# Kernel tuning notes

Measured on AMD Instinct MI355X. Metric: run time of the kernel, lower is better.

## Reference

```python
import jax, jax.numpy as jnp
import numpy as np

B, G, L, S = 4096, 16000, 64, 20000  # batch spots, genes, labels, total spots
LOG_2PI = float(np.log(2.0 * np.pi))


def _log_nb_positive_altparam(x, r, o):
    # NB with total_count r > 0 and logits o (stereoscope parametrization)
    return (jax.lax.lgamma(x + r) - jax.lax.lgamma(r) - jax.lax.lgamma(x + 1.0)
            + x * jax.nn.log_sigmoid(o) + r * jax.nn.log_sigmoid(-o))


def setup_inputs() -> dict:
    key = jax.random.key(0)
    ks = jax.random.split(key, 8)
    x = jax.random.randint(ks[0], (B, G), 0, 100, dtype=jnp.int32)
    y = jax.random.randint(ks[1], (B, 1), 0, L, dtype=jnp.int32)
    ind_x = jax.random.randint(ks[2], (B, 1), 0, S, dtype=jnp.int32)
    W = jax.random.normal(ks[3], (G, L), dtype=jnp.float32)          # fixed dictionary
    px_o = 0.5 * jax.random.normal(ks[4], (G,), dtype=jnp.float32)   # fixed log-odds
    eta = jax.random.normal(ks[5], (G,), dtype=jnp.float32)
    V = jax.random.normal(ks[6], (L + 1, S), dtype=jnp.float32)
    beta = 0.1 * jax.random.normal(ks[7], (G,), dtype=jnp.float32)
    return {"x": x, "y": y, "ind_x": ind_x, "W": W, "px_o": px_o,
            "eta": eta, "V": V, "beta": beta}


def reference(x, y, ind_x, W, px_o, eta, V, beta):
    x_f = x.astype(jnp.float32)                      # [B, G]
    beta_sp = jax.nn.softplus(beta)                  # [G]
    w_sp = jax.nn.softplus(W)                        # [G, L]
    eps_sp = jax.nn.softplus(eta)                    # [G]
    # r_hat = [beta*W | eps]  -> [G, L+1]
    r_hat = jnp.concatenate([beta_sp[:, None] * w_sp, eps_sp[:, None]], axis=1)
    # column-gather from V (embedding lookup over spots), then softplus
    v_ind = jax.nn.softplus(V[:, ind_x[:, 0]])       # [L+1, B]
    # thin matmul, inner dim L+1; px_rate: [B, G]
    px_rate = jnp.einsum("gl,lb->bg", r_hat, v_ind)
    # NB reconstruction loss per spot
    reconst_loss = -jnp.sum(_log_nb_positive_altparam(x_f, px_rate, px_o[None, :]), axis=-1)  # [B]
    # -sum log N(eta; 0, 1)
    neg_log_likelihood_prior = jnp.sum(0.5 * LOG_2PI + 0.5 * eta * eta)
    return (reconst_loss, jnp.float32(0.0), neg_log_likelihood_prior)
```

## Files before the change

### kernel.cpp

```cpp
#include <hip/hip_runtime.h>
#include <hip/hip_bf16.h>
#include <math.h>

#define Gn 16000
#define Bn 4096
#define Ln 64
#define Sn 20000

typedef __attribute__((ext_vector_type(8))) short bf16x8;
typedef __attribute__((ext_vector_type(4))) float f32x4;


__device__ __forceinline__ float softplus_precise(float z) {
    return fmaxf(z, 0.0f) + log1pf(__expf(-fabsf(z)));
}

__device__ __forceinline__ float lgamma_pos8(float z) {
    float p = z * (z + 1.f) * (z + 2.f) * (z + 3.f)
                * (z + 4.f) * (z + 5.f) * (z + 6.f) * (z + 7.f);
    float w = z + 8.f;
    return (w - 0.5f) * __logf(w) - w + 0.9189385332046727f
           + __fdividef(1.0f, 12.0f * w) - __logf(p);
}

__device__ __forceinline__ unsigned short f2bf(float f) {
    union { float f; unsigned int u; } v; v.f = f;
    unsigned int r = v.u + 0x7fff + ((v.u >> 16) & 1);
    return (unsigned short)(r >> 16);
}


__global__ void prep_genes(const float* __restrict__ W,
                           const float* __restrict__ px_o,
                           const float* __restrict__ eta,
                           const float* __restrict__ beta,
                           unsigned short* __restrict__ rhB,
                           float* __restrict__ lsp1,
                           float* __restrict__ lsn,
                           float* __restrict__ eps) {
    int idx = blockIdx.x * 256 + threadIdx.x;
    int g = idx >> 6;
    float bsp = softplus_precise(beta[g]);
    rhB[idx] = f2bf(bsp * softplus_precise(W[idx]));
    if (idx < Gn) {
        eps[idx] = softplus_precise(eta[idx]);
        float o = px_o[idx];
        lsp1[idx] = -softplus_precise(-o) - 1.0f;
        lsn[idx]  = -softplus_precise(o);
    }
}

__global__ void prep_spots(const float* __restrict__ V,
                           const int* __restrict__ ind_x,
                           unsigned short* __restrict__ vBg,
                           float* __restrict__ v64) {
    int idx = blockIdx.x * 256 + threadIdx.x;
    int b = idx >> 6, l = idx & 63;
    int s = ind_x[b];
    vBg[idx] = f2bf(softplus_precise(V[l * Sn + s]));
    if (idx < Bn) {
        int s2 = ind_x[idx];
        v64[idx] = softplus_precise(V[Ln * Sn + s2]);
    }
}

__global__ void prior_kernel(const float* __restrict__ eta, float* __restrict__ out) {
    int idx = blockIdx.x * 256 + threadIdx.x;
    float s = 0.f;
    if (idx < Gn) {
        float e = eta[idx];
        s = 0.9189385332046727f + 0.5f * e * e;
    }
    #pragma unroll
    for (int off = 32; off; off >>= 1) s += __shfl_xor(s, off, 64);
    __shared__ float red[4];
    if ((threadIdx.x & 63) == 0) red[threadIdx.x >> 6] = s;
    __syncthreads();
    if (threadIdx.x == 0) atomicAdd(&out[Bn + 1], red[0] + red[1] + red[2] + red[3]);
}


__global__ __launch_bounds__(256) void main_kernel(
    const int*            __restrict__ x,
    const unsigned short* __restrict__ rhB,
    const unsigned short* __restrict__ vBg,
    const float*          __restrict__ v64,
    const float*          __restrict__ lsp1g,
    const float*          __restrict__ lsng,
    const float*          __restrict__ epsg,
    float*                __restrict__ out) {
    __shared__ __align__(16) unsigned short sA[64][72];
    __shared__ __align__(16) unsigned short sB[64][72];
    __shared__ float sv64[64];
    __shared__ float sLsp1[64], sLsn[64], sEps[64];
    __shared__ float lfact[100];

    const int tid = threadIdx.x;
    const int g0 = blockIdx.x * 64;
    const int b0 = blockIdx.y * 64;

    {
        int row = tid >> 3;
        int c   = (tid & 7) * 8;
        *(uint4*)&sA[row][c]      = *(const uint4*)&vBg[(b0 + row) * 64 + c];
        *(uint4*)&sA[row + 32][c] = *(const uint4*)&vBg[(b0 + row + 32) * 64 + c];
        *(uint4*)&sB[row][c]      = *(const uint4*)&rhB[(g0 + row) * 64 + c];
        *(uint4*)&sB[row + 32][c] = *(const uint4*)&rhB[(g0 + row + 32) * 64 + c];
    }
    if (tid < 64) {
        sv64[tid]  = v64[b0 + tid];
        sLsp1[tid] = lsp1g[g0 + tid];
        sLsn[tid]  = lsng[g0 + tid];
        sEps[tid]  = epsg[g0 + tid];
    }
    if (tid < 100) lfact[tid] = lgamma_pos8((float)tid + 1.0f);

    const int wave = tid >> 6, lane = tid & 63;
    const int quad = lane >> 4, ln = lane & 15;
    const int mrow  = wave * 16 + ln;
    const int brow0 = b0 + wave * 16 + quad * 4;

    int xv[4][4];
    #pragma unroll
    for (int nb = 0; nb < 4; nb++) {
        int g = g0 + nb * 16 + ln;
        #pragma unroll
        for (int r = 0; r < 4; r++)
            xv[nb][r] = x[(size_t)(brow0 + r) * Gn + g];
    }

    f32x4 acc[4];
    #pragma unroll
    for (int nb = 0; nb < 4; nb++) acc[nb] = (f32x4){0.f, 0.f, 0.f, 0.f};

    __syncthreads();

    #pragma unroll
    for (int kb = 0; kb < 2; kb++) {
        bf16x8 af = *(const bf16x8*)&sA[mrow][kb * 32 + quad * 8];
        #pragma unroll
        for (int nb = 0; nb < 4; nb++) {
            bf16x8 bfr = *(const bf16x8*)&sB[nb * 16 + ln][kb * 32 + quad * 8];
            acc[nb] = __builtin_amdgcn_mfma_f32_16x16x32_bf16(af, bfr, acc[nb], 0, 0, 0);
        }
    }

    float vvr[4];
    #pragma unroll
    for (int r = 0; r < 4; r++) vvr[r] = sv64[wave * 16 + quad * 4 + r];

    float rowpart[4] = {0.f, 0.f, 0.f, 0.f};
    #pragma unroll
    for (int nb = 0; nb < 4; nb++) {
        const float lsp1v = sLsp1[nb * 16 + ln];
        const float lsnv  = sLsn[nb * 16 + ln];
        const float ev    = sEps[nb * 16 + ln];
        #pragma unroll
        for (int r = 0; r < 4; r++) {
            const float rr = fmaf(ev, vvr[r], acc[nb][r]);
            const int   xi = xv[nb][r];
            const float xf = (float)xi;
            const float s  = rr + xf;
            float t = fmaf(s - 0.5f, __logf(s), -lfact[xi]);
            t = fmaf(-(rr - 0.5f), __logf(rr), t);
            t = fmaf(xf, lsp1v, t);
            t = fmaf(rr, lsnv, t);
            rowpart[r] += t;
        }
    }

    #pragma unroll
    for (int r = 0; r < 4; r++) {
        float v = rowpart[r];
        v += __shfl_xor(v, 1, 64);
        v += __shfl_xor(v, 2, 64);
        v += __shfl_xor(v, 4, 64);
        v += __shfl_xor(v, 8, 64);
        if (ln == 0) atomicAdd(&out[brow0 + r], -v);
    }
}


extern "C" void kernel_launch(void* const* d_in, const int* in_sizes, int n_in,
                              void* d_out, int out_size, void* d_ws, size_t ws_size,
                              hipStream_t stream) {
    const int*   x     = (const int*)d_in[0];
    const int*   ind_x = (const int*)d_in[2];
    const float* W     = (const float*)d_in[3];
    const float* px_o  = (const float*)d_in[4];
    const float* eta   = (const float*)d_in[5];
    const float* V     = (const float*)d_in[6];
    const float* beta  = (const float*)d_in[7];
    float* out = (float*)d_out;

    char* wsb = (char*)d_ws;
    unsigned short* rhB  = (unsigned short*)(wsb);
    unsigned short* vBg  = (unsigned short*)(wsb + 2048000);
    float*          v64  = (float*)(wsb + 2572288);
    float*          lsp1 = (float*)(wsb + 2588672);
    float*          lsn  = (float*)(wsb + 2652672);
    float*          eps  = (float*)(wsb + 2716672);

    hipMemsetAsync(d_out, 0, (Bn + 2) * sizeof(float), stream);

    prep_genes<<<(Gn * 64) / 256, 256, 0, stream>>>(W, px_o, eta, beta, rhB, lsp1, lsn, eps);
    prep_spots<<<(Bn * 64) / 256, 256, 0, stream>>>(V, ind_x, vBg, v64);
    prior_kernel<<<(Gn + 255) / 256, 256, 0, stream>>>(eta, out);

    dim3 grid(Gn / 64, Bn / 64);
    main_kernel<<<grid, 256, 0, stream>>>(x, rhB, vBg, v64, lsp1, lsn, eps, out);
}
```

Before: 436.2 us.

## Stage x tiles through LDS with vector loads and replace atomics with partial-sum reduction

The main kernel now loads the 64x64 x tile with coalesced int4 loads into shared memory instead of strided scalar per-lane global reads. Each block writes its per-row partial sums to a workspace buffer rather than issuing many atomicAdds to the output. A separate reduce kernel then sums the 250 gene-block partials per spot, using ten chunks with a few atomics each. The aim is better global load efficiency and less atomic contention, at the cost of extra LDS use, a block barrier, a 4 MB partial buffer and another kernel launch.

```diff
diff --git a/kernel.cpp b/kernel.cpp
--- a/kernel.cpp
+++ b/kernel.cpp
@@ -6,6 +6,7 @@
 #define Bn 4096
 #define Ln 64
 #define Sn 20000
+#define NGB 250
 
 typedef __attribute__((ext_vector_type(8))) short bf16x8;
 typedef __attribute__((ext_vector_type(4))) float f32x4;
@@ -88,17 +89,29 @@
     const float*          __restrict__ lsp1g,
     const float*          __restrict__ lsng,
     const float*          __restrict__ epsg,
-    float*                __restrict__ out) {
+    float*                __restrict__ partial) {
     __shared__ __align__(16) unsigned short sA[64][72];
     __shared__ __align__(16) unsigned short sB[64][72];
+    __shared__ __align__(16) int sX[64 * 68];
     __shared__ float sv64[64];
     __shared__ float sLsp1[64], sLsn[64], sEps[64];
     __shared__ float lfact[100];
+    __shared__ float pred[64];
 
     const int tid = threadIdx.x;
     const int g0 = blockIdx.x * 64;
     const int b0 = blockIdx.y * 64;
 
+    {
+        int trow = tid >> 4;
+        int tcol = (tid & 15) * 4;
+        #pragma unroll
+        for (int p = 0; p < 4; p++) {
+            int row = p * 16 + trow;
+            int4 v = *(const int4*)&x[(size_t)(b0 + row) * Gn + g0 + tcol];
+            *(int4*)&sX[row * 68 + tcol] = v;
+        }
+    }
     {
         int row = tid >> 3;
         int c   = (tid & 7) * 8;
@@ -117,17 +130,8 @@
 
     const int wave = tid >> 6, lane = tid & 63;
     const int quad = lane >> 4, ln = lane & 15;
-    const int mrow  = wave * 16 + ln;
-    const int brow0 = b0 + wave * 16 + quad * 4;
-
-    int xv[4][4];
-    #pragma unroll
-    for (int nb = 0; nb < 4; nb++) {
-        int g = g0 + nb * 16 + ln;
-        #pragma unroll
-        for (int r = 0; r < 4; r++)
-            xv[nb][r] = x[(size_t)(brow0 + r) * Gn + g];
-    }
+    const int mrow = wave * 16 + ln;
+    const int xrow = wave * 16 + quad * 4;
 
     f32x4 acc[4];
     #pragma unroll
@@ -147,7 +151,7 @@
 
     float vvr[4];
     #pragma unroll
-    for (int r = 0; r < 4; r++) vvr[r] = sv64[wave * 16 + quad * 4 + r];
+    for (int r = 0; r < 4; r++) vvr[r] = sv64[xrow + r];
 
     float rowpart[4] = {0.f, 0.f, 0.f, 0.f};
     #pragma unroll
@@ -158,7 +162,7 @@
         #pragma unroll
         for (int r = 0; r < 4; r++) {
             const float rr = fmaf(ev, vvr[r], acc[nb][r]);
-            const int   xi = xv[nb][r];
+            const int   xi = sX[(xrow + r) * 68 + nb * 16 + ln];
             const float xf = (float)xi;
             const float s  = rr + xf;
             float t = fmaf(s - 0.5f, __logf(s), -lfact[xi]);
@@ -176,8 +180,26 @@
         v += __shfl_xor(v, 2, 64);
         v += __shfl_xor(v, 4, 64);
         v += __shfl_xor(v, 8, 64);
-        if (ln == 0) atomicAdd(&out[brow0 + r], -v);
-    }
+        if (ln == 0) pred[xrow + r] = v;
+    }
+    __syncthreads();
+    if (tid < 64) partial[(size_t)blockIdx.x * Bn + b0 + tid] = pred[tid];
+}
+
+__global__ __launch_bounds__(256) void reduce_kernel(const float* __restrict__ partial,
+                                                     float* __restrict__ out) {
+    int b = blockIdx.x * 256 + threadIdx.x;
+    int gc0 = blockIdx.y * 25;
+    float s0 = 0.f, s1 = 0.f, s2 = 0.f, s3 = 0.f, s4 = 0.f;
+    #pragma unroll
+    for (int i = 0; i < 25; i += 5) {
+        s0 += partial[(size_t)(gc0 + i + 0) * Bn + b];
+        s1 += partial[(size_t)(gc0 + i + 1) * Bn + b];
+        s2 += partial[(size_t)(gc0 + i + 2) * Bn + b];
+        s3 += partial[(size_t)(gc0 + i + 3) * Bn + b];
+        s4 += partial[(size_t)(gc0 + i + 4) * Bn + b];
+    }
+    atomicAdd(&out[b], -(s0 + s1 + s2 + s3 + s4));
 }
 
 
@@ -200,6 +222,7 @@
     float*          lsp1 = (float*)(wsb + 2588672);
     float*          lsn  = (float*)(wsb + 2652672);
     float*          eps  = (float*)(wsb + 2716672);
+    float*          part = (float*)(wsb + 2780672);
 
     hipMemsetAsync(d_out, 0, (Bn + 2) * sizeof(float), stream);
 
@@ -207,6 +230,9 @@
     prep_spots<<<(Bn * 64) / 256, 256, 0, stream>>>(V, ind_x, vBg, v64);
     prior_kernel<<<(Gn + 255) / 256, 256, 0, stream>>>(eta, out);
 
-    dim3 grid(Gn / 64, Bn / 64);
-    main_kernel<<<grid, 256, 0, stream>>>(x, rhB, vBg, v64, lsp1, lsn, eps, out);
-}
+    dim3 grid(NGB, Bn / 64);
+    main_kernel<<<grid, 256, 0, stream>>>(x, rhB, vBg, v64, lsp1, lsn, eps, part);
+
+    dim3 rgrid(Bn / 256, 10);
+    reduce_kernel<<<rgrid, 256, 0, stream>>>(part, out);
+}
```

Result: faster. 394.0 us (-9.7%).

## Make main kernel persistent over gene tiles with double-buffered async LDS loads

Applied to the files above, without the earlier changes.

Each block now keeps its spot tile's A fragments in registers and walks 10 consecutive 64-gene tiles. The x tile and the rhB tile for the next step are staged into swizzled LDS buffers with global_load_lds while the current tile is computed. Per-gene constants are packed into one float4, and the per-row atomics are replaced with a partial-sum buffer plus a separate reduce kernel. The aim is to hide x load latency and amortise setup and atomic costs. In exchange the grid is much smaller (25x64 blocks), which may underfill the GPU, and LDS use per block goes up.

```diff
diff --git a/kernel.cpp b/kernel.cpp
--- a/kernel.cpp
+++ b/kernel.cpp
@@ -6,6 +6,8 @@
 #define Bn 4096
 #define Ln 64
 #define Sn 20000
+#define NSPLIT 25
+#define ITERS 10
 
 typedef __attribute__((ext_vector_type(8))) short bf16x8;
 typedef __attribute__((ext_vector_type(4))) float f32x4;
@@ -29,24 +31,32 @@
     return (unsigned short)(r >> 16);
 }
 
+__device__ __forceinline__ void load_lds16(const void* gsrc, void* lds) {
+    __builtin_amdgcn_global_load_lds(
+        (const __attribute__((address_space(1))) unsigned int*)gsrc,
+        (__attribute__((address_space(3))) unsigned int*)lds,
+        16, 0, 0);
+}
+
 
 __global__ void prep_genes(const float* __restrict__ W,
                            const float* __restrict__ px_o,
                            const float* __restrict__ eta,
                            const float* __restrict__ beta,
                            unsigned short* __restrict__ rhB,
-                           float* __restrict__ lsp1,
-                           float* __restrict__ lsn,
-                           float* __restrict__ eps) {
+                           float4* __restrict__ gcon) {
     int idx = blockIdx.x * 256 + threadIdx.x;
     int g = idx >> 6;
     float bsp = softplus_precise(beta[g]);
     rhB[idx] = f2bf(bsp * softplus_precise(W[idx]));
     if (idx < Gn) {
-        eps[idx] = softplus_precise(eta[idx]);
         float o = px_o[idx];
-        lsp1[idx] = -softplus_precise(-o) - 1.0f;
-        lsn[idx]  = -softplus_precise(o);
+        float4 c;
+        c.x = -softplus_precise(-o) - 1.0f;
+        c.y = -softplus_precise(o);
+        c.z = softplus_precise(eta[idx]);
+        c.w = 0.f;
+        gcon[idx] = c;
     }
 }
 
@@ -80,104 +90,128 @@
 }
 
 
-__global__ __launch_bounds__(256) void main_kernel(
+__global__ __launch_bounds__(256, 3) void main_kernel(
     const int*            __restrict__ x,
     const unsigned short* __restrict__ rhB,
     const unsigned short* __restrict__ vBg,
     const float*          __restrict__ v64,
-    const float*          __restrict__ lsp1g,
-    const float*          __restrict__ lsng,
-    const float*          __restrict__ epsg,
-    float*                __restrict__ out) {
-    __shared__ __align__(16) unsigned short sA[64][72];
-    __shared__ __align__(16) unsigned short sB[64][72];
-    __shared__ float sv64[64];
-    __shared__ float sLsp1[64], sLsn[64], sEps[64];
+    const float4*         __restrict__ gcon,
+    float*                __restrict__ partial) {
+    __shared__ __align__(16) int            sX[2][64 * 64];
+    __shared__ __align__(16) unsigned short sB[2][64 * 64];
     __shared__ float lfact[100];
-
-    const int tid = threadIdx.x;
-    const int g0 = blockIdx.x * 64;
-    const int b0 = blockIdx.y * 64;
-
-    {
-        int row = tid >> 3;
-        int c   = (tid & 7) * 8;
-        *(uint4*)&sA[row][c]      = *(const uint4*)&vBg[(b0 + row) * 64 + c];
-        *(uint4*)&sA[row + 32][c] = *(const uint4*)&vBg[(b0 + row + 32) * 64 + c];
-        *(uint4*)&sB[row][c]      = *(const uint4*)&rhB[(g0 + row) * 64 + c];
-        *(uint4*)&sB[row + 32][c] = *(const uint4*)&rhB[(g0 + row + 32) * 64 + c];
-    }
-    if (tid < 64) {
-        sv64[tid]  = v64[b0 + tid];
-        sLsp1[tid] = lsp1g[g0 + tid];
-        sLsn[tid]  = lsng[g0 + tid];
-        sEps[tid]  = epsg[g0 + tid];
-    }
-    if (tid < 100) lfact[tid] = lgamma_pos8((float)tid + 1.0f);
-
+    __shared__ float pred[64];
+
+    const int tid  = threadIdx.x;
     const int wave = tid >> 6, lane = tid & 63;
     const int quad = lane >> 4, ln = lane & 15;
-    const int mrow  = wave * 16 + ln;
-    const int brow0 = b0 + wave * 16 + quad * 4;
-
-    int xv[4][4];
-    #pragma unroll
-    for (int nb = 0; nb < 4; nb++) {
-        int g = g0 + nb * 16 + ln;
-        #pragma unroll
-        for (int r = 0; r < 4; r++)
-            xv[nb][r] = x[(size_t)(brow0 + r) * Gn + g];
-    }
-
-    f32x4 acc[4];
-    #pragma unroll
-    for (int nb = 0; nb < 4; nb++) acc[nb] = (f32x4){0.f, 0.f, 0.f, 0.f};
-
+    const int b0    = blockIdx.y * 64;
+    const int gbase = blockIdx.x * ITERS;
+
+    const int mrow = wave * 16 + ln;
+    const int xrow = wave * 16 + quad * 4;
+
+    bf16x8 av[2];
+    av[0] = *(const bf16x8*)&vBg[(b0 + mrow) * 64 + 0 * 32 + quad * 8];
+    av[1] = *(const bf16x8*)&vBg[(b0 + mrow) * 64 + 1 * 32 + quad * 8];
+    float vvr[4];
+    #pragma unroll
+    for (int r = 0; r < 4; r++) vvr[r] = v64[b0 + xrow + r];
+
+    if (tid < 100) lfact[tid] = lgamma_pos8((float)tid + 1.0f);
+
+#define STAGE(buf, gb) do {                                                        \
+        const int g0s = (gb) * 64;                                                 \
+        _Pragma("unroll")                                                          \
+        for (int c = 0; c < 4; c++) {                                              \
+            int rowc = wave * 16 + c * 4 + (lane >> 4);                            \
+            int slot = (lane & 15) ^ (rowc & 7);                                   \
+            load_lds16(&x[(size_t)(b0 + rowc) * Gn + g0s + slot * 4],              \
+                       &sX[buf][(wave * 16 + c * 4) * 64]);                        \
+        }                                                                          \
+        _Pragma("unroll")                                                          \
+        for (int c = 0; c < 2; c++) {                                              \
+            int rowc = wave * 16 + c * 8 + (lane >> 3);                            \
+            int slot = (lane & 7) ^ (rowc & 7);                                    \
+            load_lds16(&rhB[(size_t)(g0s + rowc) * 64 + slot * 8],                 \
+                       &sB[buf][(wave * 16 + c * 8) * 64]);                        \
+        }                                                                          \
+    } while (0)
+
+    STAGE(0, gbase);
     __syncthreads();
 
-    #pragma unroll
-    for (int kb = 0; kb < 2; kb++) {
-        bf16x8 af = *(const bf16x8*)&sA[mrow][kb * 32 + quad * 8];
+    float rowacc[4] = {0.f, 0.f, 0.f, 0.f};
+
+    for (int t = 0; t < ITERS; ++t) {
+        const int cur = t & 1;
+        if (t + 1 < ITERS) STAGE(cur ^ 1, gbase + t + 1);
+
+        const int g0 = (gbase + t) * 64;
+
+        float4 cc[4];
+        #pragma unroll
+        for (int nb = 0; nb < 4; nb++) cc[nb] = gcon[g0 + nb * 16 + ln];
+
+        f32x4 acc[4];
+        #pragma unroll
+        for (int nb = 0; nb < 4; nb++) acc[nb] = (f32x4){0.f, 0.f, 0.f, 0.f};
+        #pragma unroll
+        for (int kb = 0; kb < 2; kb++) {
+            #pragma unroll
+            for (int nb = 0; nb < 4; nb++) {
+                const int nbr = nb * 16 + ln;
+                const int boff = nbr * 128 + ((kb * 64 + quad * 16) ^ ((nbr & 7) << 4));
+                bf16x8 bfr = *(const bf16x8*)((const char*)&sB[cur][0] + boff);
+                acc[nb] = __builtin_amdgcn_mfma_f32_16x16x32_bf16(av[kb], bfr, acc[nb], 0, 0, 0);
+            }
+        }
+
         #pragma unroll
         for (int nb = 0; nb < 4; nb++) {
-            bf16x8 bfr = *(const bf16x8*)&sB[nb * 16 + ln][kb * 32 + quad * 8];
-            acc[nb] = __builtin_amdgcn_mfma_f32_16x16x32_bf16(af, bfr, acc[nb], 0, 0, 0);
+            const float lsp1v = cc[nb].x;
+            const float lsnv  = cc[nb].y;
+            const float ev    = cc[nb].z;
+            #pragma unroll
+            for (int r = 0; r < 4; r++) {
+                const int   row = xrow + r;
+                const int   dcol = (nb * 16 + ln) ^ ((row & 7) << 2);
+                const int   xi = sX[cur][row * 64 + dcol];
+                const float rr = fmaf(ev, vvr[r], acc[nb][r]);
+                const float xf = (float)xi;
+                const float s  = rr + xf;
+                float tt = fmaf(s - 0.5f, __logf(s), -lfact[xi]);
+                tt = fmaf(-(rr - 0.5f), __logf(rr), tt);
+                tt = fmaf(xf, lsp1v, tt);
+                tt = fmaf(rr, lsnv, tt);
+                rowacc[r] += tt;
+            }
         }
-    }
-
-    float vvr[4];
-    #pragma unroll
-    for (int r = 0; r < 4; r++) vvr[r] = sv64[wave * 16 + quad * 4 + r];
-
-    float rowpart[4] = {0.f, 0.f, 0.f, 0.f};
-    #pragma unroll
-    for (int nb = 0; nb < 4; nb++) {
-        const float lsp1v = sLsp1[nb * 16 + ln];
-        const float lsnv  = sLsn[nb * 16 + ln];
-        const float ev    = sEps[nb * 16 + ln];
-        #pragma unroll
-        for (int r = 0; r < 4; r++) {
-            const float rr = fmaf(ev, vvr[r], acc[nb][r]);
-            const int   xi = xv[nb][r];
-            const float xf = (float)xi;
-            const float s  = rr + xf;
-            float t = fmaf(s - 0.5f, __logf(s), -lfact[xi]);
-            t = fmaf(-(rr - 0.5f), __logf(rr), t);
-            t = fmaf(xf, lsp1v, t);
-            t = fmaf(rr, lsnv, t);
-            rowpart[r] += t;
-        }
-    }
+
+        __syncthreads();
+    }
+#undef STAGE
 
     #pragma unroll
     for (int r = 0; r < 4; r++) {
-        float v = rowpart[r];
+        float v = rowacc[r];
         v += __shfl_xor(v, 1, 64);
         v += __shfl_xor(v, 2, 64);
         v += __shfl_xor(v, 4, 64);
         v += __shfl_xor(v, 8, 64);
-        if (ln == 0) atomicAdd(&out[brow0 + r], -v);
-    }
+        if (ln == 0) pred[xrow + r] = v;
+    }
+    __syncthreads();
+    if (tid < 64) partial[(size_t)blockIdx.x * Bn + b0 + tid] = pred[tid];
+}
+
+__global__ __launch_bounds__(256) void reduce_kernel(const float* __restrict__ partial,
+                                                     float* __restrict__ out) {
+    int b = blockIdx.x * 256 + threadIdx.x;
+    float s = 0.f;
+    #pragma unroll
+    for (int i = 0; i < NSPLIT; i++) s += partial[(size_t)i * Bn + b];
+    out[b] = -s;
 }
 
 
@@ -197,16 +231,17 @@
     unsigned short* rhB  = (unsigned short*)(wsb);
     unsigned short* vBg  = (unsigned short*)(wsb + 2048000);
     float*          v64  = (float*)(wsb + 2572288);
-    float*          lsp1 = (float*)(wsb + 2588672);
-    float*          lsn  = (float*)(wsb + 2652672);
-    float*          eps  = (float*)(wsb + 2716672);
+    float4*         gcon = (float4*)(wsb + 2588672);
+    float*          part = (float*)(wsb + 2844672);
 
     hipMemsetAsync(d_out, 0, (Bn + 2) * sizeof(float), stream);
 
-    prep_genes<<<(Gn * 64) / 256, 256, 0, stream>>>(W, px_o, eta, beta, rhB, lsp1, lsn, eps);
+    prep_genes<<<(Gn * 64) / 256, 256, 0, stream>>>(W, px_o, eta, beta, rhB, gcon);
     prep_spots<<<(Bn * 64) / 256, 256, 0, stream>>>(V, ind_x, vBg, v64);
     prior_kernel<<<(Gn + 255) / 256, 256, 0, stream>>>(eta, out);
 
-    dim3 grid(Gn / 64, Bn / 64);
-    main_kernel<<<grid, 256, 0, stream>>>(x, rhB, vBg, v64, lsp1, lsn, eps, out);
-}
+    dim3 grid(NSPLIT, Bn / 64);
+    main_kernel<<<grid, 256, 0, stream>>>(x, rhB, vBg, v64, gcon, part);
+
+    reduce_kernel<<<Bn / 256, 256, 0, stream>>>(part, out);
+}
```

Measured after the change: 414.6 us. 1.05x faster.

## Replace per-row atomics with partial-sum buffer and separate reduction kernel

Applied to the files above, without the earlier changes.

Each main-kernel block now writes its 64 per-spot partial sums to a workspace buffer indexed by gene tile, and a new reduce kernel sums the 250 gene-tile partials per spot. This removes the atomic contention on the output rows. The grid is transposed so spot tiles vary fastest, and the prior reduction is folded into prep_genes so one kernel launch goes away. The cost is an extra 4 MB of partial traffic and one additional kernel launch for the reduction.

```diff
diff --git a/kernel.cpp b/kernel.cpp
--- a/kernel.cpp
+++ b/kernel.cpp
@@ -6,6 +6,7 @@
 #define Bn 4096
 #define Ln 64
 #define Sn 20000
+#define NGT 250
 
 typedef __attribute__((ext_vector_type(8))) short bf16x8;
 typedef __attribute__((ext_vector_type(4))) float f32x4;
@@ -37,16 +38,29 @@
                            unsigned short* __restrict__ rhB,
                            float* __restrict__ lsp1,
                            float* __restrict__ lsn,
-                           float* __restrict__ eps) {
+                           float* __restrict__ eps,
+                           float* __restrict__ out) {
     int idx = blockIdx.x * 256 + threadIdx.x;
     int g = idx >> 6;
     float bsp = softplus_precise(beta[g]);
     rhB[idx] = f2bf(bsp * softplus_precise(W[idx]));
+    float s = 0.f;
     if (idx < Gn) {
         eps[idx] = softplus_precise(eta[idx]);
         float o = px_o[idx];
         lsp1[idx] = -softplus_precise(-o) - 1.0f;
         lsn[idx]  = -softplus_precise(o);
+        float e = eta[idx];
+        s = 0.9189385332046727f + 0.5f * e * e;
+    }
+    #pragma unroll
+    for (int off = 32; off; off >>= 1) s += __shfl_xor(s, off, 64);
+    __shared__ float red[4];
+    if ((threadIdx.x & 63) == 0) red[threadIdx.x >> 6] = s;
+    __syncthreads();
+    if (threadIdx.x == 0) {
+        float t = red[0] + red[1] + red[2] + red[3];
+        if (t != 0.f) atomicAdd(&out[Bn + 1], t);
     }
 }
 
@@ -64,21 +78,6 @@
     }
 }
 
-__global__ void prior_kernel(const float* __restrict__ eta, float* __restrict__ out) {
-    int idx = blockIdx.x * 256 + threadIdx.x;
-    float s = 0.f;
-    if (idx < Gn) {
-        float e = eta[idx];
-        s = 0.9189385332046727f + 0.5f * e * e;
-    }
-    #pragma unroll
-    for (int off = 32; off; off >>= 1) s += __shfl_xor(s, off, 64);
-    __shared__ float red[4];
-    if ((threadIdx.x & 63) == 0) red[threadIdx.x >> 6] = s;
-    __syncthreads();
-    if (threadIdx.x == 0) atomicAdd(&out[Bn + 1], red[0] + red[1] + red[2] + red[3]);
-}
-
 
 __global__ __launch_bounds__(256) void main_kernel(
     const int*            __restrict__ x,
@@ -88,16 +87,17 @@
     const float*          __restrict__ lsp1g,
     const float*          __restrict__ lsng,
     const float*          __restrict__ epsg,
-    float*                __restrict__ out) {
+    float*                __restrict__ partial) {
     __shared__ __align__(16) unsigned short sA[64][72];
     __shared__ __align__(16) unsigned short sB[64][72];
     __shared__ float sv64[64];
     __shared__ float sLsp1[64], sLsn[64], sEps[64];
     __shared__ float lfact[100];
+    __shared__ float pred[64];
 
     const int tid = threadIdx.x;
-    const int g0 = blockIdx.x * 64;
-    const int b0 = blockIdx.y * 64;
+    const int b0 = blockIdx.x * 64;
+    const int g0 = blockIdx.y * 64;
 
     {
         int row = tid >> 3;
@@ -176,8 +176,24 @@
         v += __shfl_xor(v, 2, 64);
         v += __shfl_xor(v, 4, 64);
         v += __shfl_xor(v, 8, 64);
-        if (ln == 0) atomicAdd(&out[brow0 + r], -v);
-    }
+        if (ln == 0) pred[wave * 16 + quad * 4 + r] = v;
+    }
+    __syncthreads();
+    if (tid < 64) partial[(size_t)blockIdx.y * Bn + b0 + tid] = pred[tid];
+}
+
+__global__ __launch_bounds__(256) void reduce_kernel(const float* __restrict__ partial,
+                                                     float* __restrict__ out) {
+    int b = blockIdx.x * 256 + threadIdx.x;
+    float s0 = 0.f, s1 = 0.f, s2 = 0.f, s3 = 0.f, s4 = 0.f;
+    for (int i = 0; i < NGT; i += 5) {
+        s0 += partial[(size_t)(i + 0) * Bn + b];
+        s1 += partial[(size_t)(i + 1) * Bn + b];
+        s2 += partial[(size_t)(i + 2) * Bn + b];
+        s3 += partial[(size_t)(i + 3) * Bn + b];
+        s4 += partial[(size_t)(i + 4) * Bn + b];
+    }
+    out[b] = -(s0 + s1 + s2 + s3 + s4);
 }
 
 
@@ -200,13 +216,15 @@
     float*          lsp1 = (float*)(wsb + 2588672);
     float*          lsn  = (float*)(wsb + 2652672);
     float*          eps  = (float*)(wsb + 2716672);
+    float*          part = (float*)(wsb + 2780672);
 
     hipMemsetAsync(d_out, 0, (Bn + 2) * sizeof(float), stream);
 
-    prep_genes<<<(Gn * 64) / 256, 256, 0, stream>>>(W, px_o, eta, beta, rhB, lsp1, lsn, eps);
+    prep_genes<<<(Gn * 64) / 256, 256, 0, stream>>>(W, px_o, eta, beta, rhB, lsp1, lsn, eps, out);
     prep_spots<<<(Bn * 64) / 256, 256, 0, stream>>>(V, ind_x, vBg, v64);
-    prior_kernel<<<(Gn + 255) / 256, 256, 0, stream>>>(eta, out);
-
-    dim3 grid(Gn / 64, Bn / 64);
-    main_kernel<<<grid, 256, 0, stream>>>(x, rhB, vBg, v64, lsp1, lsn, eps, out);
-}
+
+    dim3 grid(Bn / 64, Gn / 64);
+    main_kernel<<<grid, 256, 0, stream>>>(x, rhB, vBg, v64, lsp1, lsn, eps, part);
+
+    reduce_kernel<<<Bn / 256, 256, 0, stream>>>(part, out);
+}
```

After: 413.0 us. 1.06x faster.
